# Optimization experiments

Hardware: AMD Instinct MI355X
Metric: run time of the kernel (lower is better)

## Reference

```python
import jax, jax.numpy as jnp
import numpy as np

B, V, C = 32, 50, 64
E, H, A = 256, 256, 128
VOCAB = 20000
L = 10
BIG = 1e20


def setup_inputs() -> dict:
    key = jax.random.key(0)
    ks = jax.random.split(key, 16)
    pad = jax.random.bernoulli(ks[0], 0.2, (B, V, C))
    codes = jnp.where(pad, 0, jax.random.randint(ks[1], (B, V, C), 1, VOCAB + 1))
    mask = pad.astype(jnp.float32) * BIG           # 0 = real code, 1e20 = padding
    tvals = jax.random.uniform(ks[2], (B, V), jnp.float32) * 10.0  # elapsed time per visit
    emb_table = (jax.random.normal(ks[3], (VOCAB + 1, E), jnp.float32)).at[0].set(0.0)  # padding_idx=0
    s = 0.05
    WQ1 = jax.random.normal(ks[4], (A, E), jnp.float32) * s
    WK1 = jax.random.normal(ks[5], (A, E), jnp.float32) * s
    decay = jnp.full((VOCAB + 1,), -0.1, jnp.float32)
    initial = jnp.full((VOCAB + 1,), 1.0, jnp.float32)
    w_ih_f = jax.random.normal(ks[6], (4 * H, E), jnp.float32) * s
    w_hh_f = jax.random.normal(ks[7], (4 * H, H), jnp.float32) * s
    b_ih_f = jax.random.normal(ks[8], (4 * H,), jnp.float32) * s
    b_hh_f = jax.random.normal(ks[9], (4 * H,), jnp.float32) * s
    w_ih_b = jax.random.normal(ks[10], (4 * H, E), jnp.float32) * s
    w_hh_b = jax.random.normal(ks[11], (4 * H, H), jnp.float32) * s
    b_ih_b = jax.random.normal(ks[12], (4 * H,), jnp.float32) * s
    b_hh_b = jax.random.normal(ks[13], (4 * H,), jnp.float32) * s
    W_out = jax.random.normal(ks[14], (L, 2 * H), jnp.float32) * s
    b_out = jax.random.normal(ks[15], (L,), jnp.float32) * s
    return {"codes": codes, "mask": mask, "tvals": tvals, "Mode": 0,
            "emb_table": emb_table, "WQ1": WQ1, "WK1": WK1,
            "decay": decay, "initial": initial,
            "w_ih_f": w_ih_f, "w_hh_f": w_hh_f, "b_ih_f": b_ih_f, "b_hh_f": b_hh_f,
            "w_ih_b": w_ih_b, "w_hh_b": w_hh_b, "b_ih_b": b_ih_b, "b_hh_b": b_hh_b,
            "W_out": W_out, "b_out": b_out}


def _lstm(xs, w_ih, w_hh, b_ih, b_hh):
    # xs: [T, B, E] -> hs: [T, B, H]; PyTorch gate order i, f, g, o
    Hd = w_hh.shape[1]
    def step(carry, x):
        h, c = carry
        gates = x @ w_ih.T + b_ih + h @ w_hh.T + b_hh
        i, f, g, o = jnp.split(gates, 4, axis=-1)
        c = jax.nn.sigmoid(f) * c + jax.nn.sigmoid(i) * jnp.tanh(g)
        h = jax.nn.sigmoid(o) * jnp.tanh(c)
        return (h, c), h
    z = jnp.zeros((xs.shape[1], Hd), xs.dtype)
    _, hs = jax.lax.scan(step, (z, z), xs)
    return hs


def reference(codes, mask, tvals, Mode, emb_table, WQ1, WK1, decay, initial,
              w_ih_f, w_hh_f, b_ih_f, b_hh_f, w_ih_b, w_hh_b, b_ih_b, b_hh_b,
              W_out, b_out):
    b, v, c = codes.shape
    flat = codes.reshape(b * v, c)                    # [BV, C]
    emb = emb_table[flat]                             # [BV, C, E] (dropout in eval mode = identity)
    Q = jnp.einsum('nce,ae->nca', emb, WQ1)           # [BV, C, A]
    K = jnp.einsum('nce,ae->nca', emb, WK1)
    d = jnp.einsum('nca,nda->ncd', Q, K).reshape(b, v, c, c)
    d = d - mask[:, :, None, :] - mask[:, :, :, None]  # additive visit mask on rows and cols
    attn_dim = WQ1.shape[0]
    s = jax.nn.softmax(d / np.sqrt(attn_dim), axis=-1).reshape(b * v, c, c)
    f = jnp.einsum('ncd,nde->nce', s, emb)            # [BV, C, E]
    keep = ((mask - BIG) / -BIG).reshape(b * v, c, 1)  # 1 for real codes, 0 for padding
    f = keep * f
    mydecay = decay[flat]                             # [BV, C]
    myini = initial[flat]
    gate = jax.nn.sigmoid(mydecay * tvals.reshape(b * v, 1) + myini)  # [BV, C]
    vv = jnp.einsum('nc,nce->ne', gate, f).reshape(b, v, -1)
    vv = jnp.transpose(vv, (1, 0, 2))                 # [V, B, E]
    hs_f = _lstm(vv, w_ih_f, w_hh_f, b_ih_f, b_hh_f)
    hs_b = _lstm(vv[::-1], w_ih_b, w_hh_b, b_ih_b, b_hh_b)[::-1]
    last = jnp.concatenate([hs_f[-1], hs_b[-1]], axis=-1)  # [B, 2H]
    logits = last @ W_out.T + b_out
    return jax.nn.softmax(logits, axis=-1)
```

## Files before the change

### kernel.cpp

```cpp
#include <hip/hip_runtime.h>
#include <hip/hip_bf16.h>
#include <math.h>

#define Bb 32
#define Vv 50
#define Cc 64
#define Ee 256
#define Aa 128
#define Hh 256
#define Ll 10
#define BVn (Bb*Vv)
#define SCALE 0.08838834764831845f

#define NB 8
#define HS 32
#define RWS (4*HS)
#define WPAD 264
#define GPAD 132
#define CPAD 36
#define NREC 2048
#define RBUFB 32768

#define EPAD 264
#define QPAD 136

typedef __bf16 bf16x8 __attribute__((ext_vector_type(8)));
typedef float  f32x4  __attribute__((ext_vector_type(4)));
typedef unsigned u32x4 __attribute__((ext_vector_type(4)));

__device__ __forceinline__ float sigmoidf_(float x) {
    return 1.0f / (1.0f + __expf(-x));
}
__device__ __forceinline__ float tanhf_(float x) {
    return 1.0f - 2.0f / (__expf(2.0f * x) + 1.0f);
}

__global__ __launch_bounds__(256) void wsplit(
    const float* __restrict__ wq, const float* __restrict__ wk,
    __bf16* __restrict__ qh, __bf16* __restrict__ ql,
    __bf16* __restrict__ kh, __bf16* __restrict__ kl,
    u32x4* __restrict__ hrec)
{
    if (blockIdx.x < 16) {
        int g = blockIdx.x * 256 + threadIdx.x;
        u32x4 z = {0u, 0u, 0u, 0u};
        char* dst = (char*)hrec + (size_t)g * 16;
        asm volatile("global_store_dwordx4 %0, %1, off sc0 sc1"
                     :: "v"(dst), "v"(z) : "memory");
    }
    int i = blockIdx.x * 256 + threadIdx.x;
    if (i < 32768) {
        float f = wq[i];
        __bf16 h = (__bf16)f;
        qh[i] = h; ql[i] = (__bf16)(f - (float)h);
    } else {
        int j = i - 32768;
        float f = wk[j];
        __bf16 h = (__bf16)f;
        kh[j] = h; kl[j] = (__bf16)(f - (float)h);
    }
}

__global__ __launch_bounds__(256, 2) void attn_v2(
    const int*   __restrict__ codes,
    const float* __restrict__ mask,
    const float* __restrict__ tvals,
    const float* __restrict__ emb_table,
    const __bf16* __restrict__ wqhi, const __bf16* __restrict__ wqlo,
    const __bf16* __restrict__ wkhi, const __bf16* __restrict__ wklo,
    const float* __restrict__ decay,
    const float* __restrict__ initial,
    float*       __restrict__ vv)
{
    __shared__ __align__(16) __bf16 buf[4 * Cc * QPAD];
    __shared__ int   codes_l[Cc];
    __shared__ float maskcol_s[Cc], coef_s[Cc], wsum_s[Cc];
    __shared__ float wpart[4][Cc];

    __bf16* ehi = buf;
    __bf16* elo = buf + Cc * EPAD;
    __bf16* qhi = buf;
    __bf16* qlo = buf + 1 * Cc * QPAD;
    __bf16* khi = buf + 2 * Cc * QPAD;
    __bf16* klo = buf + 3 * Cc * QPAD;

    const int n   = blockIdx.x;
    const int tid = threadIdx.x;
    const int b   = n / Vv;
    const int v   = n - b * Vv;
    const int wv  = tid >> 6;
    const int lane = tid & 63;
    const int lr  = lane & 15;
    const int lq  = lane >> 4;

    if (tid < Cc) {
        codes_l[tid]   = codes[n * Cc + tid];
        maskcol_s[tid] = mask[n * Cc + tid];
    }
    __syncthreads();

    for (int i = tid; i < Cc * Ee; i += 256) {
        int c = i >> 8, e = i & 255;
        float f = emb_table[(size_t)codes_l[c] * Ee + e];
        __bf16 h = (__bf16)f;
        ehi[c * EPAD + e] = h;
        elo[c * EPAD + e] = (__bf16)(f - (float)h);
    }
    if (tid < Cc) {
        int code = codes_l[tid];
        float keep = (maskcol_s[tid] == 0.0f) ? 1.0f : 0.0f;
        coef_s[tid] = keep * sigmoidf_(decay[code] * tvals[n] + initial[code]);
    }
    __syncthreads();

    const __bf16* bh = (wv < 2) ? wqhi : wkhi;
    const __bf16* bl = (wv < 2) ? wqlo : wklo;
    const int colbase = (wv & 1) * 64;

    f32x4 acc[4][4] = {};
    for (int kt = 0; kt < 8; ++kt) {
        const int k0 = kt * 32 + lq * 8;
        bf16x8 Ahh[4], All[4], Bhh[4], Bll[4];
#pragma unroll
        for (int mf = 0; mf < 4; ++mf) {
            Ahh[mf] = *(const bf16x8*)&ehi[(mf * 16 + lr) * EPAD + k0];
            All[mf] = *(const bf16x8*)&elo[(mf * 16 + lr) * EPAD + k0];
        }
#pragma unroll
        for (int nf = 0; nf < 4; ++nf) {
            const int row = colbase + nf * 16 + lr;
            Bhh[nf] = *(const bf16x8*)&bh[row * Ee + k0];
            Bll[nf] = *(const bf16x8*)&bl[row * Ee + k0];
        }
#pragma unroll
        for (int mf = 0; mf < 4; ++mf)
#pragma unroll
            for (int nf = 0; nf < 4; ++nf) {
                acc[mf][nf] = __builtin_amdgcn_mfma_f32_16x16x32_bf16(Ahh[mf], Bhh[nf], acc[mf][nf], 0, 0, 0);
                acc[mf][nf] = __builtin_amdgcn_mfma_f32_16x16x32_bf16(Ahh[mf], Bll[nf], acc[mf][nf], 0, 0, 0);
                acc[mf][nf] = __builtin_amdgcn_mfma_f32_16x16x32_bf16(All[mf], Bhh[nf], acc[mf][nf], 0, 0, 0);
            }
    }
    __syncthreads();

    {
        __bf16* dh = (wv < 2) ? qhi : khi;
        __bf16* dl = (wv < 2) ? qlo : klo;
#pragma unroll
        for (int mf = 0; mf < 4; ++mf)
#pragma unroll
            for (int nf = 0; nf < 4; ++nf) {
                const int colb = colbase + nf * 16 + lr;
#pragma unroll
                for (int r = 0; r < 4; ++r) {
                    const int m = mf * 16 + lq * 4 + r;
                    float q = acc[mf][nf][r];
                    __bf16 h = (__bf16)q;
                    dh[m * QPAD + colb] = h;
                    dl[m * QPAD + colb] = (__bf16)(q - (float)h);
                }
            }
    }
    __syncthreads();

    f32x4 dacc[4] = {};
    for (int kt = 0; kt < 4; ++kt) {
        const int k0 = kt * 32 + lq * 8;
        bf16x8 Ahh = *(const bf16x8*)&qhi[(wv * 16 + lr) * QPAD + k0];
        bf16x8 All = *(const bf16x8*)&qlo[(wv * 16 + lr) * QPAD + k0];
#pragma unroll
        for (int nf = 0; nf < 4; ++nf) {
            bf16x8 Bhh = *(const bf16x8*)&khi[(nf * 16 + lr) * QPAD + k0];
            bf16x8 Bll = *(const bf16x8*)&klo[(nf * 16 + lr) * QPAD + k0];
            dacc[nf] = __builtin_amdgcn_mfma_f32_16x16x32_bf16(Ahh, Bhh, dacc[nf], 0, 0, 0);
            dacc[nf] = __builtin_amdgcn_mfma_f32_16x16x32_bf16(Ahh, Bll, dacc[nf], 0, 0, 0);
            dacc[nf] = __builtin_amdgcn_mfma_f32_16x16x32_bf16(All, Bhh, dacc[nf], 0, 0, 0);
        }
    }

    float p[4][4], inv[4];
#pragma unroll
    for (int r = 0; r < 4; ++r) {
#pragma unroll
        for (int nf = 0; nf < 4; ++nf)
            p[r][nf] = (dacc[nf][r] - maskcol_s[nf * 16 + lr]) * SCALE;
        float mx = fmaxf(fmaxf(p[r][0], p[r][1]), fmaxf(p[r][2], p[r][3]));
        mx = fmaxf(mx, __shfl_xor(mx, 1));
        mx = fmaxf(mx, __shfl_xor(mx, 2));
        mx = fmaxf(mx, __shfl_xor(mx, 4));
        mx = fmaxf(mx, __shfl_xor(mx, 8));
        float s = 0.f;
#pragma unroll
        for (int nf = 0; nf < 4; ++nf) { p[r][nf] = __expf(p[r][nf] - mx); s += p[r][nf]; }
        s += __shfl_xor(s, 1);
        s += __shfl_xor(s, 2);
        s += __shfl_xor(s, 4);
        s += __shfl_xor(s, 8);
        inv[r] = 1.0f / s;
    }

    float part[4];
#pragma unroll
    for (int nf = 0; nf < 4; ++nf) {
        float a = 0.f;
#pragma unroll
        for (int r = 0; r < 4; ++r) {
            const int row = wv * 16 + lq * 4 + r;
            a = fmaf(coef_s[row] * inv[r], p[r][nf], a);
        }
        part[nf] = a;
    }
#pragma unroll
    for (int nf = 0; nf < 4; ++nf) {
        part[nf] += __shfl_xor(part[nf], 16);
        part[nf] += __shfl_xor(part[nf], 32);
    }
    if (lq == 0)
#pragma unroll
        for (int nf = 0; nf < 4; ++nf) wpart[wv][nf * 16 + lr] = part[nf];
    __syncthreads();
    if (tid < Cc)
        wsum_s[tid] = wpart[0][tid] + wpart[1][tid] + wpart[2][tid] + wpart[3][tid];
    __syncthreads();

    float a3 = 0.f;
#pragma unroll 8
    for (int d = 0; d < Cc; ++d)
        a3 = fmaf(wsum_s[d], emb_table[(size_t)codes_l[d] * Ee + tid], a3);
    vv[(v * Bb + b) * Ee + tid] = a3;
}

__global__ __launch_bounds__(256) void xw_kernel(
    const float* __restrict__ vv,
    const float* __restrict__ w_ih_f, const float* __restrict__ b_ih_f,
    const float* __restrict__ b_hh_f,
    const float* __restrict__ w_ih_b, const float* __restrict__ b_ih_b,
    const float* __restrict__ b_hh_b,
    float* __restrict__ xg_f, float* __restrict__ xgb)
{
    const bool bwd = (blockIdx.x == 25);
    const float* A  = bwd ? (vv + 49 * Bb * Ee) : vv;
    const float* W  = bwd ? w_ih_b : w_ih_f;
    const float* b1 = bwd ? b_ih_b : b_ih_f;
    const float* b2 = bwd ? b_hh_b : b_hh_f;
    float* Cout     = bwd ? xgb : xg_f;
    const int M     = bwd ? Bb : BVn;
    const int m0    = bwd ? 0 : blockIdx.x * 64;
    const int j0    = blockIdx.y * 64;

    __shared__ float a_s[64 * 65];
    __shared__ float w_s[64 * 65];
    const int tid = threadIdx.x, tx = tid & 15, ty = tid >> 4;
    float acc[4][4] = {};
    for (int kc = 0; kc < 256; kc += 64) {
        __syncthreads();
        for (int idx = tid; idx < 4096; idx += 256) {
            int r = idx >> 6, kk = idx & 63;
            int m = m0 + r;
            a_s[r * 65 + kk] = (m < M) ? A[m * 256 + kc + kk] : 0.f;
            w_s[r * 65 + kk] = W[(j0 + r) * 256 + kc + kk];
        }
        __syncthreads();
#pragma unroll 8
        for (int kk = 0; kk < 64; ++kk) {
            float av[4], wv[4];
#pragma unroll
            for (int i = 0; i < 4; ++i) av[i] = a_s[(ty * 4 + i) * 65 + kk];
#pragma unroll
            for (int j = 0; j < 4; ++j) wv[j] = w_s[(tx * 4 + j) * 65 + kk];
#pragma unroll
            for (int i = 0; i < 4; ++i)
#pragma unroll
                for (int j = 0; j < 4; ++j)
                    acc[i][j] = fmaf(av[i], wv[j], acc[i][j]);
        }
    }
#pragma unroll
    for (int i = 0; i < 4; ++i) {
        int m = m0 + ty * 4 + i;
        if (m < M) {
#pragma unroll
            for (int j = 0; j < 4; ++j) {
                int jj = j0 + tx * 4 + j;
                Cout[m * 1024 + jj] = acc[i][j] + b1[jj] + b2[jj];
            }
        }
    }
}

__global__ __launch_bounds__(256) void lstm_persist(
    const float* __restrict__ xg,
    const float* __restrict__ w_hh,
    float*       __restrict__ last_f,
    u32x4*       __restrict__ hrec)
{
    __shared__ __align__(16) __bf16 w_s[RWS * WPAD];
    __shared__ __align__(16) __bf16 h_s[Bb * WPAD];
    __shared__ __align__(16) float  g_s[Bb * GPAD];
    __shared__ __align__(16) float  c_s[Bb * CPAD];

    const int tid = threadIdx.x, blk = blockIdx.x;
    const int hs0 = blk * HS;

    for (int i = tid; i < RWS * Ee; i += 256) {
        int r = i >> 8, k = i & 255;
        int grow = (r >> 5) * Hh + hs0 + (r & 31);
        w_s[r * WPAD + k] = (__bf16)w_hh[grow * Hh + k];
    }
    for (int i = tid; i < Bb * CPAD; i += 256) c_s[i] = 0.f;
    __syncthreads();

    const int l  = tid & 63, wvi = tid >> 6;
    const int lr = l & 15,   lq  = l >> 4;
    const int b_nl = tid >> 3, jg = tid & 7;
    const int col = hs0 + jg * 4;

    const float* x0 = xg + (size_t)b_nl * 1024;
    f32x4 ngi = *(const f32x4*)&x0[0 * Hh + col];
    f32x4 ngf = *(const f32x4*)&x0[1 * Hh + col];
    f32x4 ngg = *(const f32x4*)&x0[2 * Hh + col];
    f32x4 ngo = *(const f32x4*)&x0[3 * Hh + col];

    for (int t = 0; t < Vv; ++t) {
        if (t > 0) {
            const char* hb = (const char*)hrec + (size_t)(t & 1) * RBUFB;
            const char* a0 = hb + (size_t)tid * 16;
            const char* a1 = a0 + 1 * 4096;
            const char* a2 = a0 + 2 * 4096;
            const char* a3 = a0 + 3 * 4096;
            const char* a4 = a0 + 4 * 4096;
            const char* a5 = a0 + 5 * 4096;
            const char* a6 = a0 + 6 * 4096;
            const char* a7 = a0 + 7 * 4096;
            u32x4 rc[8];
            const unsigned tt = (unsigned)t;
            int guard = 0;
            bool ok;
            do {
                asm volatile(
                    "global_load_dwordx4 %0, %8, off sc0 sc1\n\t"
                    "global_load_dwordx4 %1, %9, off sc0 sc1\n\t"
                    "global_load_dwordx4 %2, %10, off sc0 sc1\n\t"
                    "global_load_dwordx4 %3, %11, off sc0 sc1\n\t"
                    "global_load_dwordx4 %4, %12, off sc0 sc1\n\t"
                    "global_load_dwordx4 %5, %13, off sc0 sc1\n\t"
                    "global_load_dwordx4 %6, %14, off sc0 sc1\n\t"
                    "global_load_dwordx4 %7, %15, off sc0 sc1\n\t"
                    "s_waitcnt vmcnt(0)"
                    : "=&v"(rc[0]), "=&v"(rc[1]), "=&v"(rc[2]), "=&v"(rc[3]),
                      "=&v"(rc[4]), "=&v"(rc[5]), "=&v"(rc[6]), "=&v"(rc[7])
                    : "v"(a0), "v"(a1), "v"(a2), "v"(a3),
                      "v"(a4), "v"(a5), "v"(a6), "v"(a7)
                    : "memory");
                ok = true;
#pragma unroll
                for (int q = 0; q < 8; ++q)
                    ok = ok & (rc[q][0] == tt) & (rc[q][3] == tt);
            } while (!ok && ++guard < (1 << 16));

#pragma unroll
            for (int q = 0; q < 8; ++q) {
                int rec = tid + 256 * q;
                unsigned long long pay =
                    ((unsigned long long)rc[q][2] << 32) | rc[q][1];
                *(unsigned long long*)&h_s[(rec >> 6) * WPAD + (rec & 63) * 4] = pay;
            }
            __syncthreads();

            f32x4 a00 = {}, a01 = {}, a10 = {}, a11 = {};
#pragma unroll
            for (int kt = 0; kt < 8; ++kt) {
                int ko = kt * 32 + lq * 8;
                bf16x8 A0 = *(const bf16x8*)&h_s[lr * WPAD + ko];
                bf16x8 A1 = *(const bf16x8*)&h_s[(16 + lr) * WPAD + ko];
                bf16x8 B0 = *(const bf16x8*)&w_s[(wvi * 32 + lr) * WPAD + ko];
                bf16x8 B1 = *(const bf16x8*)&w_s[(wvi * 32 + 16 + lr) * WPAD + ko];
                a00 = __builtin_amdgcn_mfma_f32_16x16x32_bf16(A0, B0, a00, 0, 0, 0);
                a01 = __builtin_amdgcn_mfma_f32_16x16x32_bf16(A0, B1, a01, 0, 0, 0);
                a10 = __builtin_amdgcn_mfma_f32_16x16x32_bf16(A1, B0, a10, 0, 0, 0);
                a11 = __builtin_amdgcn_mfma_f32_16x16x32_bf16(A1, B1, a11, 0, 0, 0);
            }
#pragma unroll
            for (int r = 0; r < 4; ++r) {
                int b0 = lq * 4 + r;
                g_s[b0 * GPAD + wvi * 32 + lr]             = a00[r];
                g_s[b0 * GPAD + wvi * 32 + 16 + lr]        = a01[r];
                g_s[(16 + b0) * GPAD + wvi * 32 + lr]      = a10[r];
                g_s[(16 + b0) * GPAD + wvi * 32 + 16 + lr] = a11[r];
            }
            __syncthreads();
        }

        {
            f32x4 gi = ngi, gf = ngf, gg = ngg, go = ngo;
            if (t + 1 < Vv) {
                const float* nx = xg + ((size_t)(t + 1) * Bb + b_nl) * 1024;
                ngi = *(const f32x4*)&nx[0 * Hh + col];
                ngf = *(const f32x4*)&nx[1 * Hh + col];
                ngg = *(const f32x4*)&nx[2 * Hh + col];
                ngo = *(const f32x4*)&nx[3 * Hh + col];
            }
            if (t > 0) {
                int gb = b_nl * GPAD + jg * 4;
                gi += *(const f32x4*)&g_s[gb + 0 * HS];
                gf += *(const f32x4*)&g_s[gb + 1 * HS];
                gg += *(const f32x4*)&g_s[gb + 2 * HS];
                go += *(const f32x4*)&g_s[gb + 3 * HS];
            }
            f32x4 cv = *(const f32x4*)&c_s[b_nl * CPAD + jg * 4];
            float hnew[4];
#pragma unroll
            for (int u = 0; u < 4; ++u) {
                float iv = sigmoidf_(gi[u]);
                float fv = sigmoidf_(gf[u]);
                float gv = tanhf_(gg[u]);
                float ov = sigmoidf_(go[u]);
                float cn = fv * cv[u] + iv * gv;
                cv[u] = cn;
                hnew[u] = ov * tanhf_(cn);
            }
            *(f32x4*)&c_s[b_nl * CPAD + jg * 4] = cv;

            if (t < Vv - 1) {
                unsigned u0 =
                    ((unsigned)__builtin_bit_cast(unsigned short, (__bf16)hnew[0])) |
                    ((unsigned)__builtin_bit_cast(unsigned short, (__bf16)hnew[1]) << 16);
                unsigned u1 =
                    ((unsigned)__builtin_bit_cast(unsigned short, (__bf16)hnew[2])) |
                    ((unsigned)__builtin_bit_cast(unsigned short, (__bf16)hnew[3]) << 16);
                const unsigned tt1 = (unsigned)(t + 1);
                u32x4 outrec;
                outrec[0] = tt1; outrec[1] = u0; outrec[2] = u1; outrec[3] = tt1;
                char* dst = (char*)hrec + (size_t)((t + 1) & 1) * RBUFB
                          + (size_t)(b_nl * 64 + blk * 8 + jg) * 16;
                asm volatile("global_store_dwordx4 %0, %1, off sc0 sc1"
                             :: "v"(dst), "v"(outrec) : "memory");
            } else {
                f32x4 hv = {hnew[0], hnew[1], hnew[2], hnew[3]};
                *(f32x4*)&last_f[b_nl * Hh + hs0 + jg * 4] = hv;
            }
        }
    }
}

__global__ __launch_bounds__(512) void lstm_tail(
    const float* __restrict__ last_f,
    const float* __restrict__ xgb,
    const float* __restrict__ W_out,
    const float* __restrict__ b_out,
    float*       __restrict__ out)
{
    __shared__ float last_s[2 * Hh];
    __shared__ float logits_s[Ll];
    const int b = blockIdx.x, tid = threadIdx.x;

    if (tid < Hh) {
        last_s[tid] = last_f[b * Hh + tid];
    } else {
        int j = tid - Hh;
        float ig = sigmoidf_(xgb[b * 1024 + j]);
        float gg = tanhf_(xgb[b * 1024 + 2 * Hh + j]);
        float og = sigmoidf_(xgb[b * 1024 + 3 * Hh + j]);
        last_s[Hh + j] = og * tanhf_(ig * gg);
    }
    __syncthreads();

    if (tid < Ll) {
        float acc = b_out[tid];
        for (int q = 0; q < 2 * Hh; ++q)
            acc = fmaf(last_s[q], W_out[tid * 2 * Hh + q], acc);
        logits_s[tid] = acc;
    }
    __syncthreads();
    if (tid == 0) {
        float mx = -3.0e38f;
        for (int i = 0; i < Ll; ++i) mx = fmaxf(mx, logits_s[i]);
        float ex[Ll], s = 0.f;
        for (int i = 0; i < Ll; ++i) { ex[i] = __expf(logits_s[i] - mx); s += ex[i]; }
        float inv = 1.0f / s;
        for (int i = 0; i < Ll; ++i) out[b * Ll + i] = ex[i] * inv;
    }
}

extern "C" void kernel_launch(void* const* d_in, const int* in_sizes, int n_in,
                              void* d_out, int out_size, void* d_ws, size_t ws_size,
                              hipStream_t stream) {
    const int*   codes     = (const int*)  d_in[0];
    const float* mask      = (const float*)d_in[1];
    const float* tvals     = (const float*)d_in[2];
    const float* emb_table = (const float*)d_in[4];
    const float* WQ1       = (const float*)d_in[5];
    const float* WK1       = (const float*)d_in[6];
    const float* decay     = (const float*)d_in[7];
    const float* initial   = (const float*)d_in[8];
    const float* w_ih_f    = (const float*)d_in[9];
    const float* w_hh_f    = (const float*)d_in[10];
    const float* b_ih_f    = (const float*)d_in[11];
    const float* b_hh_f    = (const float*)d_in[12];
    const float* w_ih_b    = (const float*)d_in[13];
    const float* b_ih_b    = (const float*)d_in[15];
    const float* b_hh_b    = (const float*)d_in[16];
    const float* W_out     = (const float*)d_in[17];
    const float* b_out     = (const float*)d_in[18];
    float* out = (float*)d_out;

    float* ws      = (float*)d_ws;
    float* vv      = ws;
    float* xg_f    = vv + 409600;
    float* xgb     = xg_f + 1638400;
    float* last_f  = xgb + 32768;
    __bf16* wqhi   = (__bf16*)(last_f + 8192);
    __bf16* wqlo   = wqhi + 32768;
    __bf16* wkhi   = wqlo + 32768;
    __bf16* wklo   = wkhi + 32768;
    u32x4* hrec    = (u32x4*)(wklo + 32768);

    wsplit<<<256, 256, 0, stream>>>(WQ1, WK1, wqhi, wqlo, wkhi, wklo, hrec);
    attn_v2<<<BVn, 256, 0, stream>>>(codes, mask, tvals, emb_table,
                                     wqhi, wqlo, wkhi, wklo,
                                     decay, initial, vv);
    xw_kernel<<<dim3(26, 16), 256, 0, stream>>>(vv, w_ih_f, b_ih_f, b_hh_f,
                                                w_ih_b, b_ih_b, b_hh_b,
                                                xg_f, xgb);
    lstm_persist<<<NB, 256, 0, stream>>>(xg_f, w_hh_f, last_f, hrec);
    lstm_tail<<<Bb, 512, 0, stream>>>(last_f, xgb, W_out, b_out, out);
}
```

Baseline: 304.7 us.

## Port input-gate GEMM to split-bf16 MFMA, vectorize embedding split, cache LSTM weights

The FP32 shared-memory input projection GEMM becomes an MFMA kernel that splits A and W into hi/lo bf16 pairs on the fly and reads them straight from global memory, with 128-column tiles. The embedding gather in the attention kernel now does 16-byte loads and packed 8-byte stores for the hi/lo split, and a few loops get unroll pragmas. The persistent LSTM kernel loads its recurrent weight fragments into registers once instead of re-reading LDS every timestep. The trade-off is slightly lower precision in the split-bf16 GEMM (the lo*lo term is dropped) and higher register pressure in the LSTM kernel.

Result: faster. 272.5 us (median of 3 runs) (-10.6%).

```diff
diff --git a/kernel.cpp b/kernel.cpp
--- a/kernel.cpp
+++ b/kernel.cpp
@@ -33,6 +33,19 @@
 }
 __device__ __forceinline__ float tanhf_(float x) {
     return 1.0f - 2.0f / (__expf(2.0f * x) + 1.0f);
+}
+
+__device__ __forceinline__ void split8(const float* __restrict__ p,
+                                       bf16x8& hi, bf16x8& lo) {
+    f32x4 a = *(const f32x4*)p;
+    f32x4 b = *(const f32x4*)(p + 4);
+#pragma unroll
+    for (int u = 0; u < 4; ++u) {
+        __bf16 h0 = (__bf16)a[u];
+        hi[u] = h0; lo[u] = (__bf16)(a[u] - (float)h0);
+        __bf16 h1 = (__bf16)b[u];
+        hi[4 + u] = h1; lo[4 + u] = (__bf16)(b[u] - (float)h1);
+    }
 }
 
 __global__ __launch_bounds__(256) void wsplit(
@@ -99,12 +112,25 @@
     }
     __syncthreads();
 
-    for (int i = tid; i < Cc * Ee; i += 256) {
-        int c = i >> 8, e = i & 255;
-        float f = emb_table[(size_t)codes_l[c] * Ee + e];
-        __bf16 h = (__bf16)f;
-        ehi[c * EPAD + e] = h;
-        elo[c * EPAD + e] = (__bf16)(f - (float)h);
+    for (int i = tid; i < Cc * 64; i += 256) {
+        int c = i >> 6, e4 = i & 63;
+        f32x4 f = *(const f32x4*)&emb_table[(size_t)codes_l[c] * Ee + e4 * 4];
+        unsigned short hh[4], ll[4];
+#pragma unroll
+        for (int u = 0; u < 4; ++u) {
+            __bf16 h = (__bf16)f[u];
+            hh[u] = __builtin_bit_cast(unsigned short, h);
+            ll[u] = __builtin_bit_cast(unsigned short,
+                                       (__bf16)(f[u] - (float)h));
+        }
+        unsigned long long hp =
+            (unsigned long long)hh[0] | ((unsigned long long)hh[1] << 16) |
+            ((unsigned long long)hh[2] << 32) | ((unsigned long long)hh[3] << 48);
+        unsigned long long lp =
+            (unsigned long long)ll[0] | ((unsigned long long)ll[1] << 16) |
+            ((unsigned long long)ll[2] << 32) | ((unsigned long long)ll[3] << 48);
+        *(unsigned long long*)&ehi[c * EPAD + e4 * 4] = hp;
+        *(unsigned long long*)&elo[c * EPAD + e4 * 4] = lp;
     }
     if (tid < Cc) {
         int code = codes_l[tid];
@@ -118,6 +144,7 @@
     const int colbase = (wv & 1) * 64;
 
     f32x4 acc[4][4] = {};
+#pragma unroll 2
     for (int kt = 0; kt < 8; ++kt) {
         const int k0 = kt * 32 + lq * 8;
         bf16x8 Ahh[4], All[4], Bhh[4], Bll[4];
@@ -164,6 +191,7 @@
     __syncthreads();
 
     f32x4 dacc[4] = {};
+#pragma unroll
     for (int kt = 0; kt < 4; ++kt) {
         const int k0 = kt * 32 + lq * 8;
         bf16x8 Ahh = *(const bf16x8*)&qhi[(wv * 16 + lr) * QPAD + k0];
@@ -230,7 +258,7 @@
     vv[(v * Bb + b) * Ee + tid] = a3;
 }
 
-__global__ __launch_bounds__(256) void xw_kernel(
+__global__ __launch_bounds__(256) void xw_mfma(
     const float* __restrict__ vv,
     const float* __restrict__ w_ih_f, const float* __restrict__ b_ih_f,
     const float* __restrict__ b_hh_f,
@@ -246,43 +274,50 @@
     float* Cout     = bwd ? xgb : xg_f;
     const int M     = bwd ? Bb : BVn;
     const int m0    = bwd ? 0 : blockIdx.x * 64;
-    const int j0    = blockIdx.y * 64;
-
-    __shared__ float a_s[64 * 65];
-    __shared__ float w_s[64 * 65];
-    const int tid = threadIdx.x, tx = tid & 15, ty = tid >> 4;
-    float acc[4][4] = {};
-    for (int kc = 0; kc < 256; kc += 64) {
-        __syncthreads();
-        for (int idx = tid; idx < 4096; idx += 256) {
-            int r = idx >> 6, kk = idx & 63;
-            int m = m0 + r;
-            a_s[r * 65 + kk] = (m < M) ? A[m * 256 + kc + kk] : 0.f;
-            w_s[r * 65 + kk] = W[(j0 + r) * 256 + kc + kk];
-        }
-        __syncthreads();
-#pragma unroll 8
-        for (int kk = 0; kk < 64; ++kk) {
-            float av[4], wv[4];
-#pragma unroll
-            for (int i = 0; i < 4; ++i) av[i] = a_s[(ty * 4 + i) * 65 + kk];
-#pragma unroll
-            for (int j = 0; j < 4; ++j) wv[j] = w_s[(tx * 4 + j) * 65 + kk];
-#pragma unroll
-            for (int i = 0; i < 4; ++i)
-#pragma unroll
-                for (int j = 0; j < 4; ++j)
-                    acc[i][j] = fmaf(av[i], wv[j], acc[i][j]);
-        }
-    }
-#pragma unroll
-    for (int i = 0; i < 4; ++i) {
-        int m = m0 + ty * 4 + i;
-        if (m < M) {
-#pragma unroll
-            for (int j = 0; j < 4; ++j) {
-                int jj = j0 + tx * 4 + j;
-                Cout[m * 1024 + jj] = acc[i][j] + b1[jj] + b2[jj];
+    const int j0    = blockIdx.y * 128;
+
+    const int tid = threadIdx.x;
+    const int wvi = tid >> 6;
+    const int lane = tid & 63;
+    const int lr = lane & 15, lq = lane >> 4;
+
+    f32x4 acc[4][2] = {};
+#pragma unroll 2
+    for (int kt = 0; kt < 8; ++kt) {
+        const int k0 = kt * 32 + lq * 8;
+        bf16x8 Ahh[4], All[4], Bhh[2], Bll[2];
+#pragma unroll
+        for (int mf = 0; mf < 4; ++mf) {
+            int arow = m0 + mf * 16 + lr;
+            if (arow >= M) arow = M - 1;
+            split8(A + (size_t)arow * Ee + k0, Ahh[mf], All[mf]);
+        }
+#pragma unroll
+        for (int nf = 0; nf < 2; ++nf) {
+            const int brow = j0 + wvi * 32 + nf * 16 + lr;
+            split8(W + (size_t)brow * Ee + k0, Bhh[nf], Bll[nf]);
+        }
+#pragma unroll
+        for (int mf = 0; mf < 4; ++mf)
+#pragma unroll
+            for (int nf = 0; nf < 2; ++nf) {
+                acc[mf][nf] = __builtin_amdgcn_mfma_f32_16x16x32_bf16(Ahh[mf], Bhh[nf], acc[mf][nf], 0, 0, 0);
+                acc[mf][nf] = __builtin_amdgcn_mfma_f32_16x16x32_bf16(Ahh[mf], Bll[nf], acc[mf][nf], 0, 0, 0);
+                acc[mf][nf] = __builtin_amdgcn_mfma_f32_16x16x32_bf16(All[mf], Bhh[nf], acc[mf][nf], 0, 0, 0);
+            }
+    }
+
+#pragma unroll
+    for (int mf = 0; mf < 4; ++mf) {
+        const int m = m0 + mf * 16 + lq * 4;
+#pragma unroll
+        for (int nf = 0; nf < 2; ++nf) {
+            const int j = j0 + wvi * 32 + nf * 16 + lr;
+            const float bb = b1[j] + b2[j];
+#pragma unroll
+            for (int r = 0; r < 4; ++r) {
+                if (m + r < M)
+                    Cout[(size_t)(m + r) * 1024 + j] = acc[mf][nf][r] + bb;
             }
         }
     }
@@ -314,6 +349,14 @@
     const int lr = l & 15,   lq  = l >> 4;
     const int b_nl = tid >> 3, jg = tid & 7;
     const int col = hs0 + jg * 4;
+
+    bf16x8 wB0[8], wB1[8];
+#pragma unroll
+    for (int kt = 0; kt < 8; ++kt) {
+        int ko = kt * 32 + lq * 8;
+        wB0[kt] = *(const bf16x8*)&w_s[(wvi * 32 + lr) * WPAD + ko];
+        wB1[kt] = *(const bf16x8*)&w_s[(wvi * 32 + 16 + lr) * WPAD + ko];
+    }
 
     const float* x0 = xg + (size_t)b_nl * 1024;
     f32x4 ngi = *(const f32x4*)&x0[0 * Hh + col];
@@ -373,12 +416,10 @@
                 int ko = kt * 32 + lq * 8;
                 bf16x8 A0 = *(const bf16x8*)&h_s[lr * WPAD + ko];
                 bf16x8 A1 = *(const bf16x8*)&h_s[(16 + lr) * WPAD + ko];
-                bf16x8 B0 = *(const bf16x8*)&w_s[(wvi * 32 + lr) * WPAD + ko];
-                bf16x8 B1 = *(const bf16x8*)&w_s[(wvi * 32 + 16 + lr) * WPAD + ko];
-                a00 = __builtin_amdgcn_mfma_f32_16x16x32_bf16(A0, B0, a00, 0, 0, 0);
-                a01 = __builtin_amdgcn_mfma_f32_16x16x32_bf16(A0, B1, a01, 0, 0, 0);
-                a10 = __builtin_amdgcn_mfma_f32_16x16x32_bf16(A1, B0, a10, 0, 0, 0);
-                a11 = __builtin_amdgcn_mfma_f32_16x16x32_bf16(A1, B1, a11, 0, 0, 0);
+                a00 = __builtin_amdgcn_mfma_f32_16x16x32_bf16(A0, wB0[kt], a00, 0, 0, 0);
+                a01 = __builtin_amdgcn_mfma_f32_16x16x32_bf16(A0, wB1[kt], a01, 0, 0, 0);
+                a10 = __builtin_amdgcn_mfma_f32_16x16x32_bf16(A1, wB0[kt], a10, 0, 0, 0);
+                a11 = __builtin_amdgcn_mfma_f32_16x16x32_bf16(A1, wB1[kt], a11, 0, 0, 0);
             }
 #pragma unroll
             for (int r = 0; r < 4; ++r) {
@@ -519,9 +560,9 @@
     attn_v2<<<BVn, 256, 0, stream>>>(codes, mask, tvals, emb_table,
                                      wqhi, wqlo, wkhi, wklo,
                                      decay, initial, vv);
-    xw_kernel<<<dim3(26, 16), 256, 0, stream>>>(vv, w_ih_f, b_ih_f, b_hh_f,
-                                                w_ih_b, b_ih_b, b_hh_b,
-                                                xg_f, xgb);
+    xw_mfma<<<dim3(26, 8), 256, 0, stream>>>(vv, w_ih_f, b_ih_f, b_hh_f,
+                                             w_ih_b, b_ih_b, b_hh_b,
+                                             xg_f, xgb);
     lstm_persist<<<NB, 256, 0, stream>>>(xg_f, w_hh_f, last_f, hrec);
     lstm_tail<<<Bb, 512, 0, stream>>>(last_f, xgb, W_out, b_out, out);
 }
```
